# Performance work log

Measured on AMD Instinct MI355X. Metric: run time of the kernel, lower is better.

The kernel has to match this reference:

```python
import jax, jax.numpy as jnp
import numpy as np

B, N, HID, E, H = 4, 256, 256, 64, 4
OUT = HID // 2          # 128
D = OUT // H            # 32
AGG = H * (2 * D + 1)   # 260 = concat(mean D, attn_sum 1, max D) per head


def setup_inputs() -> dict:
    key = jax.random.key(0)
    ks = jax.random.split(key, 7)
    s = 0.05
    return {
        "h_x": jax.random.normal(ks[0], (B, N, HID), jnp.float32),
        "h_e": jax.random.normal(ks[1], (B, N, N, E), jnp.float32),
        "h_m": jnp.ones((B, N), jnp.float32),
        "W_Q": jax.random.normal(ks[2], (OUT, HID), jnp.float32) * s,
        "W_K": jax.random.normal(ks[3], (OUT, E), jnp.float32) * s,
        "W_V": jax.random.normal(ks[4], (OUT, E), jnp.float32) * s,
        "W_R": jax.random.normal(ks[5], (OUT, AGG), jnp.float32) * s,
    }


def reference(h_x, h_e, h_m, W_Q, W_K, W_V, W_R):
    # queries from node features: [B,H,N,D]
    h_q = (h_x @ W_Q.T).reshape(B, N, H, D).transpose(0, 2, 1, 3)
    # keys/values from dense pairwise edge features: [B,H,N,N,D]
    h_k = jnp.einsum('bnme,ce->bnmc', h_e, W_K).reshape(B, N, N, H, D).transpose(0, 3, 1, 2, 4)
    h_v = jnp.einsum('bnme,ce->bnmc', h_e, W_V).reshape(B, N, N, H, D).transpose(0, 3, 1, 2, 4)
    # broadcast dot: [B,H,N,N]
    scores = jnp.einsum('bhnd,bhnmd->bhnm', h_q, h_k) / np.float32(np.sqrt(D))
    # per-node mask broadcast as [B,1,N,1] (masks query rows)
    scores = jnp.where(h_m[:, None, :, None] == 0, -jnp.inf, scores)
    # NOTE: original code softmaxes over dim=1 = HEAD axis (faithful)
    attn = jax.nn.softmax(scores, axis=1)                      # [B,H,N,N]
    attn_w = attn[..., None] * h_v                             # [B,H,N,N,D]
    aggr_sum = attn_w.sum(axis=3)                              # [B,H,N,D]
    attn_sum = attn.sum(axis=3, keepdims=True) + 1e-8          # [B,H,N,1]
    aggr_mean = aggr_sum / attn_sum
    aggr_max = attn_w.max(axis=3)                              # [B,H,N,D]
    multi = jnp.concatenate([aggr_mean, attn_sum, aggr_max], axis=-1)  # [B,H,N,2D+1]
    aggr_out = multi.transpose(0, 2, 1, 3).reshape(B, N, AGG)  # [B,N,260]
    return aggr_out @ W_R.T                                    # [B,N,OUT]
```

## Files before the change

### kernel.cpp

```cpp
#include <hip/hip_runtime.h>

constexpr int Bb   = 4;
constexpr int Nn   = 256;
constexpr int HID  = 256;
constexpr int Ee   = 64;
constexpr int Hh   = 4;
constexpr int OUTc = 128;
constexpr int Dd   = 32;
constexpr int AGG  = 260;
constexpr int REC  = 264;
constexpr int QA_LD = 264;

constexpr size_t WS_PART  = 0;
constexpr size_t WS_QBUF  = WS_PART + (size_t)Bb * Nn * 2 * REC;
constexpr size_t WS_WRT   = WS_QBUF + (size_t)Bb * Nn * OUTc;
constexpr size_t WS_FRAGV = WS_WRT + (size_t)AGG * OUTc;
constexpr size_t WS_UFRAG = WS_FRAGV + 4096;

typedef __attribute__((ext_vector_type(8))) short short8;
typedef __attribute__((ext_vector_type(4))) float floatx4;

__device__ __forceinline__ unsigned short f2bf(float f) {
    union { float f; unsigned u; } x; x.f = f;
    unsigned r = x.u + 0x7FFFu + ((x.u >> 16) & 1u);
    return (unsigned short)(r >> 16);
}

__device__ __forceinline__ short8 pack8(floatx4 f0, floatx4 f1) {
    short8 v;
    v[0] = (short)f2bf(f0[0]); v[1] = (short)f2bf(f0[1]);
    v[2] = (short)f2bf(f0[2]); v[3] = (short)f2bf(f0[3]);
    v[4] = (short)f2bf(f1[0]); v[5] = (short)f2bf(f1[1]);
    v[6] = (short)f2bf(f1[2]); v[7] = (short)f2bf(f1[3]);
    return v;
}

__global__ __launch_bounds__(256)
void eama_pre(const float* __restrict__ h_x, const float* __restrict__ W_Q,
              const float* __restrict__ W_V, const float* __restrict__ W_R,
              unsigned short* __restrict__ wfragV, float* __restrict__ W_RT,
              float* __restrict__ qbuf)
{
    __shared__ __align__(16) unsigned short sA[16 * QA_LD];
    const int tid = threadIdx.x;
    const int bid = blockIdx.x;

    if (bid < 4) {
        const int e    = bid * 256 + tid;
        const int lane = e & 63;
        const int ks   = (e >> 6) & 1;
        const int ct   = e >> 7;
        const int ncol = lane & 15, q8 = lane >> 4;
        const float* row = W_V + (ct * 16 + ncol) * Ee;
        const int k0 = ks * 32 + q8 * 8;
        floatx4 f0 = *(const floatx4*)(row + k0);
        floatx4 f1 = *(const floatx4*)(row + k0 + 4);
        *(short8*)(wfragV + (size_t)e * 8) = pack8(f0, f1);
    } else if (bid < 134) {
        const int i = (bid - 4) * 256 + tid;
        if (i < AGG * OUTc) {
            const int c = i & 127, j = i >> 7;
            W_RT[j * OUTc + c] = W_R[c * AGG + j];
        }
    } else {
        const int b0   = (bid - 134) * 16;
        const int lane = tid & 63;
        const int wv   = tid >> 6;
        const int ncol = lane & 15, q8 = lane >> 4;

        short8 bq[2][8];
        #pragma unroll
        for (int ct = 0; ct < 2; ++ct) {
            const int c = wv * 32 + ct * 16 + ncol;
            const float* row = W_Q + c * HID;
            #pragma unroll
            for (int ks = 0; ks < 8; ++ks) {
                const int k0 = ks * 32 + q8 * 8;
                floatx4 f0 = *(const floatx4*)(row + k0);
                floatx4 f1 = *(const floatx4*)(row + k0 + 4);
                bq[ct][ks] = pack8(f0, f1);
            }
        }
        #pragma unroll
        for (int i = 0; i < 2; ++i) {
            const int idx = tid + i * 256;
            const int r = idx >> 5, blk = idx & 31;
            const float* src = h_x + (size_t)(b0 + r) * HID + blk * 8;
            floatx4 f0 = *(const floatx4*)(src);
            floatx4 f1 = *(const floatx4*)(src + 4);
            *(short8*)&sA[r * QA_LD + blk * 8] = pack8(f0, f1);
        }
        __syncthreads();
        floatx4 acc[2] = {(floatx4){0,0,0,0}, (floatx4){0,0,0,0}};
        #pragma unroll
        for (int ks = 0; ks < 8; ++ks) {
            short8 a = *(const short8*)&sA[ncol * QA_LD + ks * 32 + q8 * 8];
            acc[0] = __builtin_amdgcn_mfma_f32_16x16x32_bf16(a, bq[0][ks], acc[0], 0, 0, 0);
            acc[1] = __builtin_amdgcn_mfma_f32_16x16x32_bf16(a, bq[1][ks], acc[1], 0, 0, 0);
        }
        #pragma unroll
        for (int ct = 0; ct < 2; ++ct)
            #pragma unroll
            for (int rr = 0; rr < 4; ++rr)
                qbuf[(size_t)(b0 + q8 * 4 + rr) * OUTc + wv * 32 + ct * 16 + ncol] = acc[ct][rr];
    }
}

__global__ __launch_bounds__(256)
void eama_u(const float* __restrict__ qbuf, const float* __restrict__ W_K,
            unsigned short* __restrict__ ufrag)
{
    __shared__ float sq[OUTc];
    __shared__ __align__(16) float sU[Hh][Ee];
    const int tid = threadIdx.x;
    const int bn  = blockIdx.x;
    if (tid < OUTc) sq[tid] = qbuf[bn * OUTc + tid];
    __syncthreads();
    {
        const int h = tid >> 6, e = tid & 63;
        float a0 = 0.f, a1 = 0.f;
        #pragma unroll
        for (int d = 0; d < Dd; d += 2) {
            a0 = fmaf(sq[h * Dd + d],     W_K[(h * Dd + d) * Ee + e],     a0);
            a1 = fmaf(sq[h * Dd + d + 1], W_K[(h * Dd + d + 1) * Ee + e], a1);
        }
        sU[h][e] = (a0 + a1) * 0.1767766952966369f;
    }
    __syncthreads();
    if (tid < 128) {
        const int ks = tid >> 6, l = tid & 63;
        const int nc = l & 15, q8 = l >> 4;
        short8 v = {0,0,0,0,0,0,0,0};
        if (nc < Hh) {
            const float* u = &sU[nc][ks * 32 + q8 * 8];
            floatx4 f0 = *(const floatx4*)u;
            floatx4 f1 = *(const floatx4*)(u + 4);
            v = pack8(f0, f1);
        }
        *(short8*)(ufrag + ((size_t)(bn * 2 + ks) * 64 + l) * 8) = v;
    }
}

__global__ __launch_bounds__(256, 2)
void eama_stage1(const float* __restrict__ h_e, const float* __restrict__ h_m,
                 const unsigned short* __restrict__ wfragV,
                 const unsigned short* __restrict__ ufrag,
                 float* __restrict__ wsP)
{
    __shared__ float sVS[4][OUTc];
    __shared__ float sVM[4][OUTc];
    __shared__ float sAS[4][Hh];

    const int tid  = threadIdx.x;
    const int lane = tid & 63;
    const int w    = tid >> 6;
    const int ncol = lane & 15;
    const int q8   = lane >> 4;
    const int bn   = blockIdx.x;
    const int hf   = blockIdx.y;
    const float maskv = h_m[bn];

    short8 bfV[8][2];
    #pragma unroll
    for (int ct = 0; ct < 8; ++ct)
        #pragma unroll
        for (int ks = 0; ks < 2; ++ks)
            bfV[ct][ks] = *(const short8*)(wfragV + ((size_t)(ct * 2 + ks) * 64 + lane) * 8);
    short8 bu[2];
    bu[0] = *(const short8*)(ufrag + ((size_t)(bn * 2 + 0) * 64 + lane) * 8);
    bu[1] = *(const short8*)(ufrag + ((size_t)(bn * 2 + 1) * 64 + lane) * 8);

    float vs[8], vm[8], asum = 0.f;
    #pragma unroll
    for (int ct = 0; ct < 8; ++ct) { vs[ct] = 0.f; vm[ct] = -3.402823466e38f; }

    const float* heb = h_e + (size_t)bn * Nn * Ee;

    #pragma unroll
    for (int it = 0; it < 2; ++it) {
        const int m0 = hf * 128 + w * 32 + it * 16;
        const float* ar = heb + (size_t)(m0 + ncol) * Ee;
        short8 af[2];
        #pragma unroll
        for (int ks = 0; ks < 2; ++ks) {
            floatx4 f0 = *(const floatx4*)(ar + ks * 32 + q8 * 8);
            floatx4 f1 = *(const floatx4*)(ar + ks * 32 + q8 * 8 + 4);
            af[ks] = pack8(f0, f1);
        }
        floatx4 accV[8], accS = (floatx4){0,0,0,0};
        #pragma unroll
        for (int ct = 0; ct < 8; ++ct) accV[ct] = (floatx4){0,0,0,0};
        #pragma unroll
        for (int ks = 0; ks < 2; ++ks) {
            #pragma unroll
            for (int ct = 0; ct < 8; ++ct)
                accV[ct] = __builtin_amdgcn_mfma_f32_16x16x32_bf16(af[ks], bfV[ct][ks], accV[ct], 0, 0, 0);
            accS = __builtin_amdgcn_mfma_f32_16x16x32_bf16(af[ks], bu[ks], accS, 0, 0, 0);
        }
        float a[4];
        #pragma unroll
        for (int r = 0; r < 4; ++r) {
            float s = (maskv != 0.f) ? accS[r] : -1e30f;
            float m1 = fmaxf(s, __shfl_xor(s, 1, 64));
            m1 = fmaxf(m1, __shfl_xor(m1, 2, 64));
            float e = __expf(s - m1);
            float t = e + __shfl_xor(e, 1, 64);
            t += __shfl_xor(t, 2, 64);
            a[r] = e / t;
        }
        asum += a[0] + a[1] + a[2] + a[3];
        #pragma unroll
        for (int h = 0; h < Hh; ++h) {
            const int src = (lane & 48) | h;
            float aw0 = __shfl(a[0], src, 64);
            float aw1 = __shfl(a[1], src, 64);
            float aw2 = __shfl(a[2], src, 64);
            float aw3 = __shfl(a[3], src, 64);
            #pragma unroll
            for (int g = 0; g < 2; ++g) {
                const int ct = h * 2 + g;
                float p0 = aw0 * accV[ct][0];
                float p1 = aw1 * accV[ct][1];
                float p2 = aw2 * accV[ct][2];
                float p3 = aw3 * accV[ct][3];
                vs[ct] += (p0 + p1) + (p2 + p3);
                vm[ct] = fmaxf(vm[ct], fmaxf(fmaxf(p0, p1), fmaxf(p2, p3)));
            }
        }
    }

    #pragma unroll
    for (int ct = 0; ct < 8; ++ct) {
        vs[ct] += __shfl_xor(vs[ct], 16, 64);
        vs[ct] += __shfl_xor(vs[ct], 32, 64);
        vm[ct] = fmaxf(vm[ct], __shfl_xor(vm[ct], 16, 64));
        vm[ct] = fmaxf(vm[ct], __shfl_xor(vm[ct], 32, 64));
    }
    asum += __shfl_xor(asum, 16, 64);
    asum += __shfl_xor(asum, 32, 64);

    if (lane < 16) {
        #pragma unroll
        for (int ct = 0; ct < 8; ++ct) {
            sVS[w][ct * 16 + lane] = vs[ct];
            sVM[w][ct * 16 + lane] = vm[ct];
        }
    }
    if (lane < Hh) sAS[w][lane] = asum;
    __syncthreads();
    if (tid < OUTc) {
        const size_t base = (size_t)(bn * 2 + hf) * REC;
        float vsum = (sVS[0][tid] + sVS[1][tid]) + (sVS[2][tid] + sVS[3][tid]);
        float vmax = fmaxf(fmaxf(sVS[0][tid], sVS[0][tid]), 0.f);
        vmax = fmaxf(fmaxf(sVM[0][tid], sVM[1][tid]), fmaxf(sVM[2][tid], sVM[3][tid]));
        wsP[base + tid]        = vsum;
        wsP[base + OUTc + tid] = vmax;
        if (tid < Hh)
            wsP[base + 2 * OUTc + tid] =
                (sAS[0][tid] + sAS[1][tid]) + (sAS[2][tid] + sAS[3][tid]);
    }
}

__global__ __launch_bounds__(128)
void eama_stage2(const float* __restrict__ wsP, const float* __restrict__ W_RT,
                 float* __restrict__ out)
{
    __shared__ __align__(16) float sM[REC];
    __shared__ float sAs[Hh];
    const int tid = threadIdx.x;
    const int bn  = blockIdx.x;
    const size_t base = (size_t)bn * 2 * REC;

    float vsum = wsP[base + tid] + wsP[base + REC + tid];
    float vmax = fmaxf(wsP[base + OUTc + tid], wsP[base + REC + OUTc + tid]);
    if (tid < Hh)
        sAs[tid] = wsP[base + 2 * OUTc + tid] + wsP[base + REC + 2 * OUTc + tid] + 1e-8f;
    __syncthreads();
    {
        const int h = tid >> 5, d = tid & 31;
        sM[h * 65 + d]      = vsum / sAs[h];
        sM[h * 65 + 33 + d] = vmax;
        if (tid < Hh) sM[tid * 65 + 32] = sAs[tid];
    }
    __syncthreads();
    {
        float a0 = 0.f, a1 = 0.f, a2 = 0.f, a3 = 0.f;
        #pragma unroll 5
        for (int j = 0; j < AGG; j += 4) {
            a0 = fmaf(sM[j],     W_RT[(j)     * OUTc + tid], a0);
            a1 = fmaf(sM[j + 1], W_RT[(j + 1) * OUTc + tid], a1);
            a2 = fmaf(sM[j + 2], W_RT[(j + 2) * OUTc + tid], a2);
            a3 = fmaf(sM[j + 3], W_RT[(j + 3) * OUTc + tid], a3);
        }
        out[bn * OUTc + tid] = (a0 + a1) + (a2 + a3);
    }
}

extern "C" void kernel_launch(void* const* d_in, const int* in_sizes, int n_in,
                              void* d_out, int out_size, void* d_ws, size_t ws_size,
                              hipStream_t stream) {
    const float* h_x = (const float*)d_in[0];
    const float* h_e = (const float*)d_in[1];
    const float* h_m = (const float*)d_in[2];
    const float* W_Q = (const float*)d_in[3];
    const float* W_K = (const float*)d_in[4];
    const float* W_V = (const float*)d_in[5];
    const float* W_R = (const float*)d_in[6];
    float* out = (float*)d_out;

    float* ws            = (float*)d_ws;
    float* wsP           = ws + WS_PART;
    float* qbuf          = ws + WS_QBUF;
    float* W_RT          = ws + WS_WRT;
    unsigned short* wfV  = (unsigned short*)(ws + WS_FRAGV);
    unsigned short* ufr  = (unsigned short*)(ws + WS_UFRAG);

    eama_pre<<<dim3(198), dim3(256), 0, stream>>>(h_x, W_Q, W_V, W_R, wfV, W_RT, qbuf);
    eama_u<<<dim3(Bb * Nn), dim3(256), 0, stream>>>(qbuf, W_K, ufr);
    eama_stage1<<<dim3(Bb * Nn, 2), dim3(256), 0, stream>>>(h_e, h_m, wfV, ufr, wsP);
    eama_stage2<<<dim3(Bb * Nn), dim3(128), 0, stream>>>(wsP, W_RT, out);
}
```

Before: 129.9 us.

## Fuse stage1 and stage2 into one 512-thread block per node, split Q weight packing

Merges the two-half stage1 and the stage2 output projection into a single kernel where one 512-thread block covers all 256 edges of a node and does the W_R projection in-block. This removes the partial-result workspace round trip and one launch. W_Q bf16 fragment packing moves into the pack kernel, and the Q projection becomes its own kernel that loads the prepacked fragments, which adds a launch. Occupancy changes to one 512-thread block per CU slot, and the grid is halved.

```diff
diff --git a/kernel.cpp b/kernel.cpp
--- a/kernel.cpp
+++ b/kernel.cpp
@@ -11,11 +11,11 @@
 constexpr int REC  = 264;
 constexpr int QA_LD = 264;
 
-constexpr size_t WS_PART  = 0;
-constexpr size_t WS_QBUF  = WS_PART + (size_t)Bb * Nn * 2 * REC;
+constexpr size_t WS_QBUF  = 0;
 constexpr size_t WS_WRT   = WS_QBUF + (size_t)Bb * Nn * OUTc;
 constexpr size_t WS_FRAGV = WS_WRT + (size_t)AGG * OUTc;
-constexpr size_t WS_UFRAG = WS_FRAGV + 4096;
+constexpr size_t WS_FRAGQ = WS_FRAGV + 4096;
+constexpr size_t WS_UFRAG = WS_FRAGQ + 16384;
 
 typedef __attribute__((ext_vector_type(8))) short short8;
 typedef __attribute__((ext_vector_type(4))) float floatx4;
@@ -36,12 +36,11 @@
 }
 
 __global__ __launch_bounds__(256)
-void eama_pre(const float* __restrict__ h_x, const float* __restrict__ W_Q,
-              const float* __restrict__ W_V, const float* __restrict__ W_R,
-              unsigned short* __restrict__ wfragV, float* __restrict__ W_RT,
-              float* __restrict__ qbuf)
+void eama_pack(const float* __restrict__ W_Q, const float* __restrict__ W_V,
+               const float* __restrict__ W_R,
+               unsigned short* __restrict__ wfragV, unsigned short* __restrict__ wfragQ,
+               float* __restrict__ W_RT)
 {
-    __shared__ __align__(16) unsigned short sA[16 * QA_LD];
     const int tid = threadIdx.x;
     const int bid = blockIdx.x;
 
@@ -56,54 +55,68 @@
         floatx4 f0 = *(const floatx4*)(row + k0);
         floatx4 f1 = *(const floatx4*)(row + k0 + 4);
         *(short8*)(wfragV + (size_t)e * 8) = pack8(f0, f1);
-    } else if (bid < 134) {
-        const int i = (bid - 4) * 256 + tid;
+    } else if (bid < 20) {
+        const int e    = (bid - 4) * 256 + tid;
+        const int lane = e & 63;
+        const int ks   = (e >> 6) & 7;
+        const int ct   = (e >> 9) & 1;
+        const int wv   = (e >> 10) & 3;
+        const int ncol = lane & 15, q8 = lane >> 4;
+        const float* row = W_Q + (wv * 32 + ct * 16 + ncol) * HID;
+        const int k0 = ks * 32 + q8 * 8;
+        floatx4 f0 = *(const floatx4*)(row + k0);
+        floatx4 f1 = *(const floatx4*)(row + k0 + 4);
+        *(short8*)(wfragQ + (size_t)e * 8) = pack8(f0, f1);
+    } else {
+        const int i = (bid - 20) * 256 + tid;
         if (i < AGG * OUTc) {
             const int c = i & 127, j = i >> 7;
             W_RT[j * OUTc + c] = W_R[c * AGG + j];
         }
-    } else {
-        const int b0   = (bid - 134) * 16;
-        const int lane = tid & 63;
-        const int wv   = tid >> 6;
-        const int ncol = lane & 15, q8 = lane >> 4;
-
-        short8 bq[2][8];
-        #pragma unroll
-        for (int ct = 0; ct < 2; ++ct) {
-            const int c = wv * 32 + ct * 16 + ncol;
-            const float* row = W_Q + c * HID;
-            #pragma unroll
-            for (int ks = 0; ks < 8; ++ks) {
-                const int k0 = ks * 32 + q8 * 8;
-                floatx4 f0 = *(const floatx4*)(row + k0);
-                floatx4 f1 = *(const floatx4*)(row + k0 + 4);
-                bq[ct][ks] = pack8(f0, f1);
-            }
-        }
-        #pragma unroll
-        for (int i = 0; i < 2; ++i) {
-            const int idx = tid + i * 256;
-            const int r = idx >> 5, blk = idx & 31;
-            const float* src = h_x + (size_t)(b0 + r) * HID + blk * 8;
-            floatx4 f0 = *(const floatx4*)(src);
-            floatx4 f1 = *(const floatx4*)(src + 4);
-            *(short8*)&sA[r * QA_LD + blk * 8] = pack8(f0, f1);
-        }
-        __syncthreads();
-        floatx4 acc[2] = {(floatx4){0,0,0,0}, (floatx4){0,0,0,0}};
+    }
+}
+
+__global__ __launch_bounds__(256)
+void eama_qproj(const float* __restrict__ h_x, const unsigned short* __restrict__ wfragQ,
+                float* __restrict__ qbuf)
+{
+    __shared__ __align__(16) unsigned short sA[16 * QA_LD];
+    const int tid  = threadIdx.x;
+    const int b0   = blockIdx.x * 16;
+    const int lane = tid & 63;
+    const int wv   = tid >> 6;
+    const int ncol = lane & 15, q8 = lane >> 4;
+
+    short8 bq[2][8];
+    #pragma unroll
+    for (int ct = 0; ct < 2; ++ct)
         #pragma unroll
         for (int ks = 0; ks < 8; ++ks) {
-            short8 a = *(const short8*)&sA[ncol * QA_LD + ks * 32 + q8 * 8];
-            acc[0] = __builtin_amdgcn_mfma_f32_16x16x32_bf16(a, bq[0][ks], acc[0], 0, 0, 0);
-            acc[1] = __builtin_amdgcn_mfma_f32_16x16x32_bf16(a, bq[1][ks], acc[1], 0, 0, 0);
-        }
-        #pragma unroll
-        for (int ct = 0; ct < 2; ++ct)
-            #pragma unroll
-            for (int rr = 0; rr < 4; ++rr)
-                qbuf[(size_t)(b0 + q8 * 4 + rr) * OUTc + wv * 32 + ct * 16 + ncol] = acc[ct][rr];
-    }
+            const int e = ((wv * 2 + ct) * 8 + ks) * 64 + lane;
+            bq[ct][ks] = *(const short8*)(wfragQ + (size_t)e * 8);
+        }
+    #pragma unroll
+    for (int i = 0; i < 2; ++i) {
+        const int idx = tid + i * 256;
+        const int r = idx >> 5, blk = idx & 31;
+        const float* src = h_x + (size_t)(b0 + r) * HID + blk * 8;
+        floatx4 f0 = *(const floatx4*)(src);
+        floatx4 f1 = *(const floatx4*)(src + 4);
+        *(short8*)&sA[r * QA_LD + blk * 8] = pack8(f0, f1);
+    }
+    __syncthreads();
+    floatx4 acc[2] = {(floatx4){0,0,0,0}, (floatx4){0,0,0,0}};
+    #pragma unroll
+    for (int ks = 0; ks < 8; ++ks) {
+        short8 a = *(const short8*)&sA[ncol * QA_LD + ks * 32 + q8 * 8];
+        acc[0] = __builtin_amdgcn_mfma_f32_16x16x32_bf16(a, bq[0][ks], acc[0], 0, 0, 0);
+        acc[1] = __builtin_amdgcn_mfma_f32_16x16x32_bf16(a, bq[1][ks], acc[1], 0, 0, 0);
+    }
+    #pragma unroll
+    for (int ct = 0; ct < 2; ++ct)
+        #pragma unroll
+        for (int rr = 0; rr < 4; ++rr)
+            qbuf[(size_t)(b0 + q8 * 4 + rr) * OUTc + wv * 32 + ct * 16 + ncol] = acc[ct][rr];
 }
 
 __global__ __launch_bounds__(256)
@@ -141,23 +154,24 @@
     }
 }
 
-__global__ __launch_bounds__(256, 2)
-void eama_stage1(const float* __restrict__ h_e, const float* __restrict__ h_m,
-                 const unsigned short* __restrict__ wfragV,
-                 const unsigned short* __restrict__ ufrag,
-                 float* __restrict__ wsP)
+__global__ __launch_bounds__(512, 1)
+void eama_main(const float* __restrict__ h_e, const float* __restrict__ h_m,
+               const unsigned short* __restrict__ wfragV,
+               const unsigned short* __restrict__ ufrag,
+               const float* __restrict__ W_RT, float* __restrict__ out)
 {
-    __shared__ float sVS[4][OUTc];
-    __shared__ float sVM[4][OUTc];
-    __shared__ float sAS[4][Hh];
+    __shared__ float sVS[8][OUTc];
+    __shared__ float sVM[8][OUTc];
+    __shared__ float sAS[8][Hh];
+    __shared__ float sAsum[Hh];
+    __shared__ __align__(16) float sM[REC];
+    __shared__ float sAcc[4][OUTc];
 
     const int tid  = threadIdx.x;
     const int lane = tid & 63;
     const int w    = tid >> 6;
     const int ncol = lane & 15;
-    const int q8   = lane >> 4;
     const int bn   = blockIdx.x;
-    const int hf   = blockIdx.y;
     const float maskv = h_m[bn];
 
     short8 bfV[8][2];
@@ -175,10 +189,11 @@
     for (int ct = 0; ct < 8; ++ct) { vs[ct] = 0.f; vm[ct] = -3.402823466e38f; }
 
     const float* heb = h_e + (size_t)bn * Nn * Ee;
+    const int q8 = lane >> 4;
 
     #pragma unroll
     for (int it = 0; it < 2; ++it) {
-        const int m0 = hf * 128 + w * 32 + it * 16;
+        const int m0 = w * 32 + it * 16;
         const float* ar = heb + (size_t)(m0 + ncol) * Ee;
         short8 af[2];
         #pragma unroll
@@ -248,52 +263,38 @@
     }
     if (lane < Hh) sAS[w][lane] = asum;
     __syncthreads();
+    if (tid < Hh) {
+        float a = 1e-8f;
+        #pragma unroll
+        for (int ww = 0; ww < 8; ++ww) a += sAS[ww][tid];
+        sAsum[tid] = a;
+    }
+    __syncthreads();
     if (tid < OUTc) {
-        const size_t base = (size_t)(bn * 2 + hf) * REC;
-        float vsum = (sVS[0][tid] + sVS[1][tid]) + (sVS[2][tid] + sVS[3][tid]);
-        float vmax = fmaxf(fmaxf(sVS[0][tid], sVS[0][tid]), 0.f);
-        vmax = fmaxf(fmaxf(sVM[0][tid], sVM[1][tid]), fmaxf(sVM[2][tid], sVM[3][tid]));
-        wsP[base + tid]        = vsum;
-        wsP[base + OUTc + tid] = vmax;
-        if (tid < Hh)
-            wsP[base + 2 * OUTc + tid] =
-                (sAS[0][tid] + sAS[1][tid]) + (sAS[2][tid] + sAS[3][tid]);
-    }
-}
-
-__global__ __launch_bounds__(128)
-void eama_stage2(const float* __restrict__ wsP, const float* __restrict__ W_RT,
-                 float* __restrict__ out)
-{
-    __shared__ __align__(16) float sM[REC];
-    __shared__ float sAs[Hh];
-    const int tid = threadIdx.x;
-    const int bn  = blockIdx.x;
-    const size_t base = (size_t)bn * 2 * REC;
-
-    float vsum = wsP[base + tid] + wsP[base + REC + tid];
-    float vmax = fmaxf(wsP[base + OUTc + tid], wsP[base + REC + OUTc + tid]);
-    if (tid < Hh)
-        sAs[tid] = wsP[base + 2 * OUTc + tid] + wsP[base + REC + 2 * OUTc + tid] + 1e-8f;
+        float vsum = 0.f, vmax = -3.402823466e38f;
+        #pragma unroll
+        for (int ww = 0; ww < 8; ++ww) {
+            vsum += sVS[ww][tid];
+            vmax = fmaxf(vmax, sVM[ww][tid]);
+        }
+        const int h = tid >> 5, d = tid & 31;
+        sM[h * 65 + d]      = vsum / sAsum[h];
+        sM[h * 65 + 33 + d] = vmax;
+        if (tid < Hh) sM[tid * 65 + 32] = sAsum[tid];
+    }
     __syncthreads();
     {
-        const int h = tid >> 5, d = tid & 31;
-        sM[h * 65 + d]      = vsum / sAs[h];
-        sM[h * 65 + 33 + d] = vmax;
-        if (tid < Hh) sM[tid * 65 + 32] = sAs[tid];
-    }
-    __syncthreads();
-    {
-        float a0 = 0.f, a1 = 0.f, a2 = 0.f, a3 = 0.f;
+        const int c = tid & 127, part = tid >> 7;
+        const int j0 = part * 65;
+        float acc = 0.f;
         #pragma unroll 5
-        for (int j = 0; j < AGG; j += 4) {
-            a0 = fmaf(sM[j],     W_RT[(j)     * OUTc + tid], a0);
-            a1 = fmaf(sM[j + 1], W_RT[(j + 1) * OUTc + tid], a1);
-            a2 = fmaf(sM[j + 2], W_RT[(j + 2) * OUTc + tid], a2);
-            a3 = fmaf(sM[j + 3], W_RT[(j + 3) * OUTc + tid], a3);
-        }
-        out[bn * OUTc + tid] = (a0 + a1) + (a2 + a3);
-    }
+        for (int j = j0; j < j0 + 65; ++j)
+            acc = fmaf(sM[j], W_RT[j * OUTc + c], acc);
+        sAcc[part][c] = acc;
+    }
+    __syncthreads();
+    if (tid < OUTc)
+        out[bn * OUTc + tid] = (sAcc[0][tid] + sAcc[1][tid]) + (sAcc[2][tid] + sAcc[3][tid]);
 }
 
 extern "C" void kernel_launch(void* const* d_in, const int* in_sizes, int n_in,
@@ -309,14 +310,14 @@
     float* out = (float*)d_out;
 
     float* ws            = (float*)d_ws;
-    float* wsP           = ws + WS_PART;
     float* qbuf          = ws + WS_QBUF;
     float* W_RT          = ws + WS_WRT;
     unsigned short* wfV  = (unsigned short*)(ws + WS_FRAGV);
+    unsigned short* wfQ  = (unsigned short*)(ws + WS_FRAGQ);
     unsigned short* ufr  = (unsigned short*)(ws + WS_UFRAG);
 
-    eama_pre<<<dim3(198), dim3(256), 0, stream>>>(h_x, W_Q, W_V, W_R, wfV, W_RT, qbuf);
+    eama_pack<<<dim3(150), dim3(256), 0, stream>>>(W_Q, W_V, W_R, wfV, wfQ, W_RT);
+    eama_qproj<<<dim3(Bb * Nn / 16), dim3(256), 0, stream>>>(h_x, wfQ, qbuf);
     eama_u<<<dim3(Bb * Nn), dim3(256), 0, stream>>>(qbuf, W_K, ufr);
-    eama_stage1<<<dim3(Bb * Nn, 2), dim3(256), 0, stream>>>(h_e, h_m, wfV, ufr, wsP);
-    eama_stage2<<<dim3(Bb * Nn), dim3(128), 0, stream>>>(wsP, W_RT, out);
-}
+    eama_main<<<dim3(Bb * Nn), dim3(512), 0, stream>>>(h_e, h_m, wfV, ufr, W_RT, out);
+}
```

New measurement: 139.8 us. +7.6%, slower.
